# Performance work log

Hardware: AMD Instinct MI355X
Metric: run time of the kernel (lower is better)

The kernel has to match this reference:

```python
import jax, jax.numpy as jnp
import numpy as np

T, B = 256, 128
VOCAB, EMB, HID, LABELS = 50257, 1024, 1024, 50


def setup_inputs() -> dict:
    key = jax.random.key(0)
    ks = jax.random.split(key, 6)
    sentence = jax.random.randint(ks[0], (T, B), 0, VOCAB)
    emb = jax.random.normal(ks[1], (VOCAB, EMB), dtype=jnp.float32) * 0.02
    W = jax.random.normal(ks[2], (EMB, 3 * HID), dtype=jnp.float32) * (1.0 / np.sqrt(EMB))
    b = jnp.zeros((3 * HID,), dtype=jnp.float32)
    Wout = jax.random.normal(ks[3], (HID, LABELS), dtype=jnp.float32) * (1.0 / np.sqrt(HID))
    bout = jnp.zeros((LABELS,), dtype=jnp.float32)
    return {"sentence": sentence, "emb": emb, "W": W, "b": b, "Wout": Wout, "bout": bout}


def reference(sentence, emb, W, b, Wout, bout):
    # Embedding lookup: [T, B, EMB]
    x = emb[sentence]
    # QRNN gate projection (window=1): [T, B, 3H]
    y = jnp.einsum('tbe,eh->tbh', x, W) + b
    z, f, o = jnp.split(y, 3, axis=-1)
    z = jnp.tanh(z)
    f = jax.nn.sigmoid(f)
    o = jax.nn.sigmoid(o)

    # fo-pool recurrence: c_t = f_t * z_t + (1 - f_t) * c_{t-1}, c_0 = 0
    def step(c, zf):
        z_t, f_t = zf
        c = f_t * z_t + (1.0 - f_t) * c
        return c, c

    c0 = jnp.zeros((B, HID), dtype=z.dtype)
    _, C = jax.lax.scan(step, c0, (z, f))
    # hidden output at last timestep: h_T = o_T * c_T
    h_last = o[-1] * C[-1]  # [B, HID]
    logits = h_last @ Wout + bout  # [B, LABELS]
    return jax.nn.log_softmax(logits, axis=-1)
```

## Files before the change

### kernel.cpp

```cpp
#include <hip/hip_runtime.h>
#include <hip/hip_bf16.h>

#define T_LEN 256
#define B_DIM 128
#define EMB 1024
#define HID 1024
#define NLAB 50
#define M_ROWS (T_LEN * B_DIM)
#define N3H 3072
#define KT 16

typedef __attribute__((ext_vector_type(8))) short short8;
typedef __attribute__((ext_vector_type(4))) float f32x4;

static __device__ __forceinline__ ushort f2b(float x) {
    unsigned u = __builtin_bit_cast(unsigned, x);
    unsigned lsb = (u >> 16) & 1u;
    u += 0x7fffu + lsb;
    return (ushort)(u >> 16);
}
static __device__ __forceinline__ float b2f(ushort u) {
    unsigned v = ((unsigned)u) << 16;
    return __builtin_bit_cast(float, v);
}
static __device__ __forceinline__ void gload16(const ushort* g, ushort* l) {
    __builtin_amdgcn_global_load_lds(
        (const __attribute__((address_space(1))) unsigned int*)g,
        (__attribute__((address_space(3))) unsigned int*)l,
        16, 0, 0);
}
static __device__ __forceinline__ float fast_sigmoid(float y) {
    return 1.f / (1.f + __expf(-y));
}
static __device__ __forceinline__ float fast_tanh(float y) {
    float e = __expf(2.f * y);
    return (e - 1.f) / (e + 1.f);
}

__global__ __launch_bounds__(256) void prep(
    const int* __restrict__ sent, const float* __restrict__ emb,
    const float* __restrict__ W,
    ushort* __restrict__ xb, ushort* __restrict__ Wt)
{
    __shared__ float tile[32][33];
    const int wg = blockIdx.x;
    if (wg < M_ROWS) {
        const int k4 = threadIdx.x * 4;
        const size_t src = (size_t)sent[wg] * EMB + k4;
        float4 v = *(const float4*)(emb + src);
        ushort4 o;
        o.x = f2b(v.x); o.y = f2b(v.y); o.z = f2b(v.z); o.w = f2b(v.w);
        *(ushort4*)(xb + (size_t)wg * EMB + k4) = o;
    } else {
        const int bx = wg - M_ROWS;
        const int n0 = (bx % 96) * 32, k0 = (bx / 96) * 32;
        const int tx = threadIdx.x & 31, ty = threadIdx.x >> 5;
#pragma unroll
        for (int j = 0; j < 32; j += 8)
            tile[ty + j][tx] = W[(size_t)(k0 + ty + j) * N3H + n0 + tx];
        __syncthreads();
#pragma unroll
        for (int j = 0; j < 32; j += 8)
            Wt[(size_t)(n0 + ty + j) * EMB + k0 + tx] = f2b(tile[tx][ty + j]);
    }
}

__global__ __launch_bounds__(256) void gemm128(
    const ushort* __restrict__ A, const ushort* __restrict__ Bt,
    const float* __restrict__ bias,
    ushort* __restrict__ zb, ushort* __restrict__ fb, ushort* __restrict__ ob)
{
    __shared__ ushort LA[128 * 64];
    __shared__ ushort LB[128 * 64];

    const int tid = threadIdx.x;
    const int lane = tid & 63;
    const int w = tid >> 6;
    const int wr = w >> 1, wc = w & 1;
    const int l15 = lane & 15, lh = lane >> 4;

    const int wg = blockIdx.x;
    const ushort *Ab, *Bb;
    const float* bptr;
    ushort* dst;
    int rowbase, colbase;
    bool use_tanh;
    if (wg < 4096) {
        const int w2 = (wg & 7) * 512 + (wg >> 3);
        const int mt = w2 >> 4, nt = w2 & 15;
        Ab = A + (size_t)mt * 128 * EMB;
        Bb = Bt + (size_t)nt * 128 * EMB;
        bptr = bias + nt * 128;
        rowbase = mt * 128;
        if (nt < 8) { dst = zb; colbase = nt * 128; use_tanh = true; }
        else        { dst = fb; colbase = (nt - 8) * 128; use_tanh = false; }
    } else {
        const int q = wg - 4096;
        Ab = A + (size_t)(M_ROWS - 128) * EMB;
        Bb = Bt + (size_t)(2048 + q * 128) * EMB;
        bptr = bias + 2048 + q * 128;
        rowbase = 0; colbase = q * 128;
        dst = ob; use_tanh = false;
    }

    const ushort* gA[4];
    const ushort* gB[4];
    int dOf[4];
#pragma unroll
    for (int q = 0; q < 4; q++) {
        const int c = q * 256 + tid;
        const int row = c >> 3;
        const int gsrc = (c & 7) ^ (row & 7);
        gA[q] = Ab + (size_t)row * EMB + gsrc * 8;
        gB[q] = Bb + (size_t)row * EMB + gsrc * 8;
        dOf[q] = c * 8;
    }

    const int swz0 = (lh ^ (l15 & 7)) * 8;
    const int swz1 = ((4 + lh) ^ (l15 & 7)) * 8;
    const int aRow = (wr * 64 + l15) * 64;
    const int bRow = (wc * 64 + l15) * 64;

    f32x4 acc[4][4] = {};

    for (int kk = 0; kk < KT; ++kk) {
        const int ko = kk * 64;
        gload16(gA[0] + ko, LA + dOf[0]);
        gload16(gA[1] + ko, LA + dOf[1]);
        gload16(gA[2] + ko, LA + dOf[2]);
        gload16(gA[3] + ko, LA + dOf[3]);
        gload16(gB[0] + ko, LB + dOf[0]);
        gload16(gB[1] + ko, LB + dOf[1]);
        gload16(gB[2] + ko, LB + dOf[2]);
        gload16(gB[3] + ko, LB + dOf[3]);
        __syncthreads();

        {
            short8 a0 = *(const short8*)&LA[aRow + swz0];
            short8 a1 = *(const short8*)&LA[aRow + 1024 + swz0];
            short8 a2 = *(const short8*)&LA[aRow + 2048 + swz0];
            short8 a3 = *(const short8*)&LA[aRow + 3072 + swz0];
            short8 b0 = *(const short8*)&LB[bRow + swz0];
            short8 b1 = *(const short8*)&LB[bRow + 1024 + swz0];
            short8 b2 = *(const short8*)&LB[bRow + 2048 + swz0];
            short8 b3 = *(const short8*)&LB[bRow + 3072 + swz0];
#pragma unroll
            for (int mi = 0; mi < 4; mi++) {
                const short8 am = (mi == 0) ? a0 : (mi == 1) ? a1 : (mi == 2) ? a2 : a3;
                acc[mi][0] = __builtin_amdgcn_mfma_f32_16x16x32_bf16(am, b0, acc[mi][0], 0, 0, 0);
                acc[mi][1] = __builtin_amdgcn_mfma_f32_16x16x32_bf16(am, b1, acc[mi][1], 0, 0, 0);
                acc[mi][2] = __builtin_amdgcn_mfma_f32_16x16x32_bf16(am, b2, acc[mi][2], 0, 0, 0);
                acc[mi][3] = __builtin_amdgcn_mfma_f32_16x16x32_bf16(am, b3, acc[mi][3], 0, 0, 0);
            }
        }
        {
            short8 a0 = *(const short8*)&LA[aRow + swz1];
            short8 a1 = *(const short8*)&LA[aRow + 1024 + swz1];
            short8 a2 = *(const short8*)&LA[aRow + 2048 + swz1];
            short8 a3 = *(const short8*)&LA[aRow + 3072 + swz1];
            short8 b0 = *(const short8*)&LB[bRow + swz1];
            short8 b1 = *(const short8*)&LB[bRow + 1024 + swz1];
            short8 b2 = *(const short8*)&LB[bRow + 2048 + swz1];
            short8 b3 = *(const short8*)&LB[bRow + 3072 + swz1];
#pragma unroll
            for (int mi = 0; mi < 4; mi++) {
                const short8 am = (mi == 0) ? a0 : (mi == 1) ? a1 : (mi == 2) ? a2 : a3;
                acc[mi][0] = __builtin_amdgcn_mfma_f32_16x16x32_bf16(am, b0, acc[mi][0], 0, 0, 0);
                acc[mi][1] = __builtin_amdgcn_mfma_f32_16x16x32_bf16(am, b1, acc[mi][1], 0, 0, 0);
                acc[mi][2] = __builtin_amdgcn_mfma_f32_16x16x32_bf16(am, b2, acc[mi][2], 0, 0, 0);
                acc[mi][3] = __builtin_amdgcn_mfma_f32_16x16x32_bf16(am, b3, acc[mi][3], 0, 0, 0);
            }
        }
        __syncthreads();
    }

#pragma unroll
    for (int mi = 0; mi < 4; mi++) {
#pragma unroll
        for (int ni = 0; ni < 4; ni++) {
            const int nb = wc * 64 + ni * 16 + l15;
            const float bv = bptr[nb];
            const int rl = wr * 64 + mi * 16 + lh * 4;
#pragma unroll
            for (int r = 0; r < 4; r++) {
                float y = acc[mi][ni][r] + bv;
                float a = use_tanh ? fast_tanh(y) : fast_sigmoid(y);
                dst[(size_t)(rowbase + rl + r) * HID + colbase + nb] = f2b(a);
            }
        }
    }
}

__global__ __launch_bounds__(256) void fo_pool(
    const unsigned* __restrict__ z32, const unsigned* __restrict__ fz32,
    const unsigned* __restrict__ o32, float* __restrict__ hbuf)
{
    const int p = blockIdx.x * 256 + threadIdx.x;
    float c0 = 0.f, c1 = 0.f;
#pragma unroll 8
    for (int t = 0; t < T_LEN; ++t) {
        unsigned zz = z32[(size_t)t * (B_DIM * HID / 2) + p];
        unsigned ff = fz32[(size_t)t * (B_DIM * HID / 2) + p];
        float z0 = b2f((ushort)(zz & 0xffffu)), z1 = b2f((ushort)(zz >> 16));
        float f0 = b2f((ushort)(ff & 0xffffu)), f1 = b2f((ushort)(ff >> 16));
        c0 += f0 * (z0 - c0);
        c1 += f1 * (z1 - c1);
    }
    unsigned oo = o32[p];
    float o0 = b2f((ushort)(oo & 0xffffu)), o1 = b2f((ushort)(oo >> 16));
    hbuf[2 * p]     = o0 * c0;
    hbuf[2 * p + 1] = o1 * c1;
}

__global__ __launch_bounds__(64) void classify(
    const float* __restrict__ hbuf, const float* __restrict__ Wout,
    const float* __restrict__ bout, float* __restrict__ out)
{
    __shared__ float hs[HID];
    const int b = blockIdx.x, l = threadIdx.x;
#pragma unroll
    for (int j = 0; j < HID; j += 64) hs[j + l] = hbuf[(size_t)b * HID + j + l];
    __syncthreads();
    float acc = -1e30f;
    if (l < NLAB) {
        float s = bout[l];
#pragma unroll 4
        for (int e = 0; e < HID; e++) s += hs[e] * Wout[(size_t)e * NLAB + l];
        acc = s;
    }
    float m = acc;
#pragma unroll
    for (int off = 32; off; off >>= 1) m = fmaxf(m, __shfl_xor(m, off));
    float ex = (l < NLAB) ? expf(acc - m) : 0.f;
    float sum = ex;
#pragma unroll
    for (int off = 32; off; off >>= 1) sum += __shfl_xor(sum, off);
    if (l < NLAB) out[(size_t)b * NLAB + l] = acc - m - logf(sum);
}

extern "C" void kernel_launch(void* const* d_in, const int* in_sizes, int n_in,
                              void* d_out, int out_size, void* d_ws, size_t ws_size,
                              hipStream_t stream) {
    const int* sent = (const int*)d_in[0];
    const float* emb = (const float*)d_in[1];
    const float* W = (const float*)d_in[2];
    const float* bias = (const float*)d_in[3];
    const float* Wout = (const float*)d_in[4];
    const float* bout = (const float*)d_in[5];
    float* out = (float*)d_out;

    ushort* xb = (ushort*)d_ws;
    ushort* Wt = xb + (size_t)M_ROWS * EMB;
    ushort* zb = Wt + (size_t)N3H * EMB;
    ushort* fb = zb + (size_t)M_ROWS * HID;
    ushort* ob = fb + (size_t)M_ROWS * HID;
    float* hb = (float*)(ob + (size_t)B_DIM * HID);

    hipLaunchKernelGGL(prep, dim3(M_ROWS + 3072), dim3(256), 0, stream,
                       sent, emb, W, xb, Wt);
    hipLaunchKernelGGL(gemm128, dim3(4096 + 8), dim3(256), 0, stream,
                       xb, Wt, bias, zb, fb, ob);
    hipLaunchKernelGGL(fo_pool, dim3(B_DIM * HID / 2 / 256), dim3(256), 0, stream,
                       (const unsigned*)zb, (const unsigned*)fb,
                       (const unsigned*)ob, hb);
    hipLaunchKernelGGL(classify, dim3(B_DIM), dim3(64), 0, stream,
                       hb, Wout, bout, out);
}
```

Measured before the change: 325.2 us.

## Fuse embedding gather and bf16 conversion into GEMM A-tile loading

Removes the separate gather pass that materialized bf16 embeddings, and instead loads fp32 embedding rows directly via sentence indices inside the GEMM, converting to bf16 before storing to LDS. This eliminates a large intermediate write and read. In exchange, A tiles are reloaded in fp32 for every N tile (more bytes), and the asynchronous global-to-LDS load is replaced by synchronous register loads plus conversion, which may expose latency in the main loop.

```diff
diff --git a/kernel.cpp b/kernel.cpp
--- a/kernel.cpp
+++ b/kernel.cpp
@@ -37,37 +37,25 @@
     return (e - 1.f) / (e + 1.f);
 }
 
-__global__ __launch_bounds__(256) void prep(
+__global__ __launch_bounds__(256) void transposeW(
+    const float* __restrict__ W, ushort* __restrict__ Wt)
+{
+    __shared__ float tile[32][33];
+    const int bx = blockIdx.x;
+    const int n0 = (bx % 96) * 32, k0 = (bx / 96) * 32;
+    const int tx = threadIdx.x & 31, ty = threadIdx.x >> 5;
+#pragma unroll
+    for (int j = 0; j < 32; j += 8)
+        tile[ty + j][tx] = W[(size_t)(k0 + ty + j) * N3H + n0 + tx];
+    __syncthreads();
+#pragma unroll
+    for (int j = 0; j < 32; j += 8)
+        Wt[(size_t)(n0 + ty + j) * EMB + k0 + tx] = f2b(tile[tx][ty + j]);
+}
+
+__global__ __launch_bounds__(256) void gemm128(
     const int* __restrict__ sent, const float* __restrict__ emb,
-    const float* __restrict__ W,
-    ushort* __restrict__ xb, ushort* __restrict__ Wt)
-{
-    __shared__ float tile[32][33];
-    const int wg = blockIdx.x;
-    if (wg < M_ROWS) {
-        const int k4 = threadIdx.x * 4;
-        const size_t src = (size_t)sent[wg] * EMB + k4;
-        float4 v = *(const float4*)(emb + src);
-        ushort4 o;
-        o.x = f2b(v.x); o.y = f2b(v.y); o.z = f2b(v.z); o.w = f2b(v.w);
-        *(ushort4*)(xb + (size_t)wg * EMB + k4) = o;
-    } else {
-        const int bx = wg - M_ROWS;
-        const int n0 = (bx % 96) * 32, k0 = (bx / 96) * 32;
-        const int tx = threadIdx.x & 31, ty = threadIdx.x >> 5;
-#pragma unroll
-        for (int j = 0; j < 32; j += 8)
-            tile[ty + j][tx] = W[(size_t)(k0 + ty + j) * N3H + n0 + tx];
-        __syncthreads();
-#pragma unroll
-        for (int j = 0; j < 32; j += 8)
-            Wt[(size_t)(n0 + ty + j) * EMB + k0 + tx] = f2b(tile[tx][ty + j]);
-    }
-}
-
-__global__ __launch_bounds__(256) void gemm128(
-    const ushort* __restrict__ A, const ushort* __restrict__ Bt,
-    const float* __restrict__ bias,
+    const ushort* __restrict__ Bt, const float* __restrict__ bias,
     ushort* __restrict__ zb, ushort* __restrict__ fb, ushort* __restrict__ ob)
 {
     __shared__ ushort LA[128 * 64];
@@ -80,15 +68,15 @@
     const int l15 = lane & 15, lh = lane >> 4;
 
     const int wg = blockIdx.x;
-    const ushort *Ab, *Bb;
+    const ushort* Bb;
     const float* bptr;
     ushort* dst;
-    int rowbase, colbase;
+    int arowbase, rowbase, colbase;
     bool use_tanh;
     if (wg < 4096) {
         const int w2 = (wg & 7) * 512 + (wg >> 3);
         const int mt = w2 >> 4, nt = w2 & 15;
-        Ab = A + (size_t)mt * 128 * EMB;
+        arowbase = mt * 128;
         Bb = Bt + (size_t)nt * 128 * EMB;
         bptr = bias + nt * 128;
         rowbase = mt * 128;
@@ -96,14 +84,14 @@
         else        { dst = fb; colbase = (nt - 8) * 128; use_tanh = false; }
     } else {
         const int q = wg - 4096;
-        Ab = A + (size_t)(M_ROWS - 128) * EMB;
+        arowbase = M_ROWS - 128;
         Bb = Bt + (size_t)(2048 + q * 128) * EMB;
         bptr = bias + 2048 + q * 128;
         rowbase = 0; colbase = q * 128;
         dst = ob; use_tanh = false;
     }
 
-    const ushort* gA[4];
+    const float* gAf[4];
     const ushort* gB[4];
     int dOf[4];
 #pragma unroll
@@ -111,7 +99,7 @@
         const int c = q * 256 + tid;
         const int row = c >> 3;
         const int gsrc = (c & 7) ^ (row & 7);
-        gA[q] = Ab + (size_t)row * EMB + gsrc * 8;
+        gAf[q] = emb + (size_t)sent[arowbase + row] * EMB + gsrc * 8;
         gB[q] = Bb + (size_t)row * EMB + gsrc * 8;
         dOf[q] = c * 8;
     }
@@ -125,14 +113,21 @@
 
     for (int kk = 0; kk < KT; ++kk) {
         const int ko = kk * 64;
-        gload16(gA[0] + ko, LA + dOf[0]);
-        gload16(gA[1] + ko, LA + dOf[1]);
-        gload16(gA[2] + ko, LA + dOf[2]);
-        gload16(gA[3] + ko, LA + dOf[3]);
         gload16(gB[0] + ko, LB + dOf[0]);
         gload16(gB[1] + ko, LB + dOf[1]);
         gload16(gB[2] + ko, LB + dOf[2]);
         gload16(gB[3] + ko, LB + dOf[3]);
+#pragma unroll
+        for (int q = 0; q < 4; q++) {
+            float4 v0 = *(const float4*)(gAf[q] + ko);
+            float4 v1 = *(const float4*)(gAf[q] + ko + 4);
+            short8 o;
+            o[0] = (short)f2b(v0.x); o[1] = (short)f2b(v0.y);
+            o[2] = (short)f2b(v0.z); o[3] = (short)f2b(v0.w);
+            o[4] = (short)f2b(v1.x); o[5] = (short)f2b(v1.y);
+            o[6] = (short)f2b(v1.z); o[7] = (short)f2b(v1.w);
+            *(short8*)(LA + dOf[q]) = o;
+        }
         __syncthreads();
 
         {
@@ -249,17 +244,15 @@
     const float* bout = (const float*)d_in[5];
     float* out = (float*)d_out;
 
-    ushort* xb = (ushort*)d_ws;
-    ushort* Wt = xb + (size_t)M_ROWS * EMB;
+    ushort* Wt = (ushort*)d_ws;
     ushort* zb = Wt + (size_t)N3H * EMB;
     ushort* fb = zb + (size_t)M_ROWS * HID;
     ushort* ob = fb + (size_t)M_ROWS * HID;
     float* hb = (float*)(ob + (size_t)B_DIM * HID);
 
-    hipLaunchKernelGGL(prep, dim3(M_ROWS + 3072), dim3(256), 0, stream,
-                       sent, emb, W, xb, Wt);
+    hipLaunchKernelGGL(transposeW, dim3(3072), dim3(256), 0, stream, W, Wt);
     hipLaunchKernelGGL(gemm128, dim3(4096 + 8), dim3(256), 0, stream,
-                       xb, Wt, bias, zb, fb, ob);
+                       sent, emb, Wt, bias, zb, fb, ob);
     hipLaunchKernelGGL(fo_pool, dim3(B_DIM * HID / 2 / 256), dim3(256), 0, stream,
                        (const unsigned*)zb, (const unsigned*)fb,
                        (const unsigned*)ob, hb);
```

Result: slower. 409.6 us (+25.9%).
